# Kernel tuning notes

Hardware: AMD Instinct MI355X
Metric: run time of the kernel (lower is better)

The kernel has to match this reference:

```python
import jax, jax.numpy as jnp
import numpy as np

NUM_HEADS = 16
SIZE_PER_HEAD = 64
HIDDEN = NUM_HEADS * SIZE_PER_HEAD  # 1024
B, F, T = 4, 1024, 1024
NEG_INF = -10000.0


def setup_inputs() -> dict:
    key = jax.random.key(0)
    ks = jax.random.split(key, 6)
    scale = 0.02
    return {
        "from_tensor": jax.random.normal(ks[0], (B, F, HIDDEN), dtype=jnp.float32),
        "to_tensor": jax.random.normal(ks[1], (B, T, HIDDEN), dtype=jnp.float32),
        "attention_mask": jnp.ones((B, F, T), dtype=jnp.float32),
        "Wq": jax.random.normal(ks[2], (HIDDEN, HIDDEN), dtype=jnp.float32) * scale,
        "bq": jnp.zeros((HIDDEN,), dtype=jnp.float32),
        "Wk": jax.random.normal(ks[3], (HIDDEN, HIDDEN), dtype=jnp.float32) * scale,
        "bk": jnp.zeros((HIDDEN,), dtype=jnp.float32),
        "Wv": jax.random.normal(ks[4], (HIDDEN, HIDDEN), dtype=jnp.float32) * scale,
        "bv": jnp.zeros((HIDDEN,), dtype=jnp.float32),
    }


def _split_heads(x, seq_len):
    # [B, S, H*Dh] -> [B, H, S, Dh]
    return x.reshape(B, seq_len, NUM_HEADS, SIZE_PER_HEAD).transpose(0, 2, 1, 3)


def reference(from_tensor, to_tensor, attention_mask, Wq, bq, Wk, bk, Wv, bv):
    # Q/K/V dense projections (query_act/key_act/value_act are None -> linear)
    q = _split_heads(from_tensor @ Wq + bq, F)   # [B,H,F,Dh]
    k = _split_heads(to_tensor @ Wk + bk, T)     # [B,H,T,Dh]
    v = _split_heads(to_tensor @ Wv + bv, T)     # [B,H,T,Dh]

    # scaled dot-product attention scores: [B,H,F,T]
    scores = jnp.einsum("bhfd,bhtd->bhft", q, k) / jnp.sqrt(
        jnp.asarray(SIZE_PER_HEAD, dtype=q.dtype))

    # BERT-style mask adder: mask==1 -> attend, mask==0 -> -10000
    adder = (1.0 - attention_mask[:, None, :, :]) * NEG_INF
    scores = scores + adder

    attention_probs = jax.nn.softmax(scores, axis=-1)  # dropout_prob=0.0

    ctx = jnp.einsum("bhft,bhtd->bhfd", attention_probs, v)  # [B,H,F,Dh]
    ctx = ctx.transpose(0, 2, 1, 3).reshape(B, F, NUM_HEADS * SIZE_PER_HEAD)
    return ctx, attention_probs
```

## Files before the change

kernel.cpp:

```cpp
#include <hip/hip_runtime.h>

typedef unsigned short u16;
typedef __bf16 bf16x8 __attribute__((ext_vector_type(8)));
typedef float f32x4 __attribute__((ext_vector_type(4)));
typedef u16 u16x8 __attribute__((ext_vector_type(8)));
typedef u16 u16x4 __attribute__((ext_vector_type(4)));

#define NUM_HEADS 16
#define HIDDEN 1024
#define BATCH 4
#define SEQ 1024
#define C1 0.1803368809109783f
#define LOG2E 1.4426950408889634f

#define VMCNT0 asm volatile("s_waitcnt vmcnt(0)" ::: "memory")

static __device__ __forceinline__ u16 f2bf(float x) {
  unsigned u = __float_as_uint(x);
  u = u + 0x7FFFu + ((u >> 16) & 1u);
  return (u16)(u >> 16);
}
static __device__ __forceinline__ float bf2f(u16 b) {
  return __uint_as_float(((unsigned)b) << 16);
}
static __device__ __forceinline__ void async16(u16* lds, const u16* g) {
  __builtin_amdgcn_global_load_lds(
      (const __attribute__((address_space(1))) void*)g,
      (__attribute__((address_space(3))) void*)lds, 16, 0, 0);
}

__global__ __launch_bounds__(256) void k_prep(
    const float* __restrict__ from, u16* __restrict__ Af,
    const float* __restrict__ to, u16* __restrict__ At,
    const float* __restrict__ Wq, const float* __restrict__ Wk,
    const float* __restrict__ Wv, u16* __restrict__ Wt,
    const float* __restrict__ mask, u16* __restrict__ adder, int* __restrict__ flags) {
  int bid = blockIdx.x;
  int tid = threadIdx.x;
  if (bid < 4096) {
    const float* in = (bid < 2048) ? from : to;
    u16* out = (bid < 2048) ? Af : At;
    int i = (bid & 2047) * 256 + tid;
    float4 a = ((const float4*)in)[i * 2];
    float4 b = ((const float4*)in)[i * 2 + 1];
    u16x8 v;
    v[0] = f2bf(a.x); v[1] = f2bf(a.y); v[2] = f2bf(a.z); v[3] = f2bf(a.w);
    v[4] = f2bf(b.x); v[5] = f2bf(b.y); v[6] = f2bf(b.z); v[7] = f2bf(b.w);
    *(u16x8*)&out[(size_t)i * 8] = v;
  } else if (bid < 4864) {
    __shared__ float tile[64][65];
    int wid = bid - 4096;
    int z = wid >> 8, rem = wid & 255;
    int x = rem & 15, y = rem >> 4;
    const float* W = (z == 0) ? Wq : (z == 1) ? Wk : Wv;
    u16* out = Wt + (size_t)z * HIDDEN * HIDDEN;
    int k0 = y * 64, n0 = x * 64;
    int r = tid >> 6, c = tid & 63;
#pragma unroll
    for (int i = 0; i < 16; ++i)
      tile[i * 4 + r][c] = W[(size_t)(k0 + i * 4 + r) * HIDDEN + n0 + c];
    __syncthreads();
#pragma unroll
    for (int i = 0; i < 16; ++i)
      out[(size_t)(n0 + i * 4 + r) * HIDDEN + k0 + c] = f2bf(tile[c][i * 4 + r]);
  } else {
    int wid = bid - 4864;
    int tt = wid & 7, ft = (wid >> 3) & 7, b = wid >> 6;
    __shared__ int sflag;
    if (tid == 0) sflag = 0;
    __syncthreads();
    size_t base = ((size_t)b * SEQ + ft * 128) * SEQ + tt * 128;
    int any = 0;
#pragma unroll
    for (int i = 0; i < 16; ++i) {
      int idx = i * 256 + tid;
      int r = idx >> 5, c4 = idx & 31;
      float4 v = *(const float4*)&mask[base + (size_t)r * SEQ + c4 * 4];
      any |= (v.x != 1.0f) | (v.y != 1.0f) | (v.z != 1.0f) | (v.w != 1.0f);
    }
    if (any) sflag = 1;
    __syncthreads();
    if (sflag) {
#pragma unroll
      for (int i = 0; i < 16; ++i) {
        int idx = i * 256 + tid;
        int r = idx >> 5, c4 = idx & 31;
        float4 v = *(const float4*)&mask[base + (size_t)r * SEQ + c4 * 4];
        u16x4 o;
        o[0] = f2bf((1.0f - v.x) * -10000.0f * LOG2E);
        o[1] = f2bf((1.0f - v.y) * -10000.0f * LOG2E);
        o[2] = f2bf((1.0f - v.z) * -10000.0f * LOG2E);
        o[3] = f2bf((1.0f - v.w) * -10000.0f * LOG2E);
        *(u16x4*)&adder[base + (size_t)r * SEQ + c4 * 4] = o;
      }
    }
    if (tid == 0) flags[(b * 8 + ft) * 8 + tt] = sflag;
  }
}

__global__ __launch_bounds__(256) void k_gemmQKV(
    const u16* __restrict__ Af, const u16* __restrict__ At,
    const u16* __restrict__ Wt,
    const float* __restrict__ bq, const float* __restrict__ bk_, const float* __restrict__ bv_,
    u16* __restrict__ Qh, u16* __restrict__ Kh, u16* __restrict__ Vt) {
  __shared__ u16 lds[3 * 128 * 64];
  int bid = blockIdx.x;
  int which = bid >> 8;
  int wg = bid & 255;
  int xcd = wg & 7, j = wg >> 3;
  int ntile = j & 7, mstrip = xcd * 4 + (j >> 3);
  int m0 = mstrip * 128, n0 = ntile * 128;
  int tid = threadIdx.x, w = tid >> 6, lane = tid & 63;
  int wr = w >> 1, wc = w & 1;
  int g = lane >> 4, cc = lane & 15;

  int sx[4], srow[4], scol[4];
#pragma unroll
  for (int i = 0; i < 4; ++i) {
    int ch = w * 4 + i;
    int x = ch * 1024 + lane * 16;
    int row = x >> 7;
    int colb = (x & 127) ^ ((row & 7) << 4);
    sx[i] = ch * 512;
    srow[i] = row;
    scol[i] = colb >> 1;
  }

  if (which == 0) {
    u16* sA = lds;
    u16* sB = lds + 8192;
    const u16* A = Af;
    const u16* B = Wt;
    f32x4 acc[4][4] = {};

    for (int kt = 0; kt < HIDDEN / 64; ++kt) {
      __syncthreads();
#pragma unroll
      for (int i = 0; i < 4; ++i) {
        async16(&sA[sx[i]], A + (size_t)(m0 + srow[i]) * HIDDEN + kt * 64 + scol[i]);
        async16(&sB[sx[i]], B + (size_t)(n0 + srow[i]) * HIDDEN + kt * 64 + scol[i]);
      }
      VMCNT0;
      __syncthreads();
#pragma unroll
      for (int kk = 0; kk < 2; ++kk) {
        bf16x8 af[4], bfr[4];
#pragma unroll
        for (int mf = 0; mf < 4; ++mf) {
          int row = wr * 64 + mf * 16 + cc;
          int colb = (kk * 64 + (g << 4)) ^ ((row & 7) << 4);
          af[mf] = *(const bf16x8*)&sA[(row * 128 + colb) >> 1];
        }
#pragma unroll
        for (int nf = 0; nf < 4; ++nf) {
          int row = wc * 64 + nf * 16 + cc;
          int colb = (kk * 64 + (g << 4)) ^ ((row & 7) << 4);
          bfr[nf] = *(const bf16x8*)&sB[(row * 128 + colb) >> 1];
        }
#pragma unroll
        for (int mf = 0; mf < 4; ++mf)
#pragma unroll
          for (int nf = 0; nf < 4; ++nf)
            acc[mf][nf] = __builtin_amdgcn_mfma_f32_16x16x32_bf16(af[mf], bfr[nf], acc[mf][nf], 0, 0, 0);
      }
    }

#pragma unroll
    for (int mf = 0; mf < 4; ++mf) {
#pragma unroll
      for (int nf = 0; nf < 4; ++nf) {
        int n = n0 + wc * 64 + nf * 16 + cc;
        float bval = bq[n];
        int h = n >> 6, d = n & 63;
#pragma unroll
        for (int r = 0; r < 4; ++r) {
          int m = m0 + wr * 64 + mf * 16 + g * 4 + r;
          int b = m >> 10, s = m & 1023;
          Qh[((((size_t)b * NUM_HEADS + h) * SEQ + s) << 6) + d] = f2bf(acc[mf][nf][r] + bval);
        }
      }
    }
  } else {
    u16* sA = lds;
    u16* sBk = lds + 8192;
    u16* sBv = lds + 16384;
    const u16* Bk = Wt + (size_t)1 * HIDDEN * HIDDEN;
    const u16* Bv = Wt + (size_t)2 * HIDDEN * HIDDEN;
    f32x4 acck[4][4] = {};
    f32x4 accv[4][4] = {};

    for (int kt = 0; kt < HIDDEN / 64; ++kt) {
      __syncthreads();
#pragma unroll
      for (int i = 0; i < 4; ++i) {
        async16(&sA[sx[i]], At + (size_t)(m0 + srow[i]) * HIDDEN + kt * 64 + scol[i]);
        async16(&sBk[sx[i]], Bk + (size_t)(n0 + srow[i]) * HIDDEN + kt * 64 + scol[i]);
        async16(&sBv[sx[i]], Bv + (size_t)(n0 + srow[i]) * HIDDEN + kt * 64 + scol[i]);
      }
      VMCNT0;
      __syncthreads();
#pragma unroll
      for (int kk = 0; kk < 2; ++kk) {
        bf16x8 af[4], bkf[4], bvf[4];
#pragma unroll
        for (int mf = 0; mf < 4; ++mf) {
          int row = wr * 64 + mf * 16 + cc;
          int colb = (kk * 64 + (g << 4)) ^ ((row & 7) << 4);
          af[mf] = *(const bf16x8*)&sA[(row * 128 + colb) >> 1];
        }
#pragma unroll
        for (int nf = 0; nf < 4; ++nf) {
          int row = wc * 64 + nf * 16 + cc;
          int colb = (kk * 64 + (g << 4)) ^ ((row & 7) << 4);
          bkf[nf] = *(const bf16x8*)&sBk[(row * 128 + colb) >> 1];
          bvf[nf] = *(const bf16x8*)&sBv[(row * 128 + colb) >> 1];
        }
#pragma unroll
        for (int mf = 0; mf < 4; ++mf)
#pragma unroll
          for (int nf = 0; nf < 4; ++nf) {
            acck[mf][nf] = __builtin_amdgcn_mfma_f32_16x16x32_bf16(af[mf], bkf[nf], acck[mf][nf], 0, 0, 0);
            accv[mf][nf] = __builtin_amdgcn_mfma_f32_16x16x32_bf16(af[mf], bvf[nf], accv[mf][nf], 0, 0, 0);
          }
      }
    }

#pragma unroll
    for (int mf = 0; mf < 4; ++mf) {
#pragma unroll
      for (int nf = 0; nf < 4; ++nf) {
        int n = n0 + wc * 64 + nf * 16 + cc;
        float bval = bk_[n];
        int h = n >> 6, d = n & 63;
#pragma unroll
        for (int r = 0; r < 4; ++r) {
          int m = m0 + wr * 64 + mf * 16 + g * 4 + r;
          int b = m >> 10, s = m & 1023;
          Kh[((((size_t)b * NUM_HEADS + h) * SEQ + s) << 6) + d] = f2bf(acck[mf][nf][r] + bval);
        }
      }
    }

    __syncthreads();
    char* T = (char*)lds;
#pragma unroll
    for (int mf = 0; mf < 4; ++mf) {
#pragma unroll
      for (int nf = 0; nf < 4; ++nf) {
        int nl = wc * 64 + nf * 16 + cc;
        float bval = bv_[n0 + nl];
        int mlb = wr * 64 + mf * 16 + g * 4;
        u16x4 v;
#pragma unroll
        for (int r = 0; r < 4; ++r) v[r] = f2bf(accv[mf][nf][r] + bval);
        int byte = nl * 256 + ((mlb * 2) ^ ((nl & 7) << 4));
        *(u16x4*)(T + byte) = v;
      }
    }
    __syncthreads();
    int nl = tid >> 1, mh = (tid & 1) * 64;
    int b = m0 >> 10, s0 = m0 & 1023;
    u16* dst = &Vt[((size_t)b * 1024 + n0 + nl) * SEQ + s0 + mh];
#pragma unroll
    for (int j2 = 0; j2 < 8; ++j2) {
      int byte = nl * 256 + (((mh + j2 * 8) * 2) ^ ((nl & 7) << 4));
      *(u16x8*)&dst[j2 * 8] = *(const u16x8*)(T + byte);
    }
  }
}

__global__ __launch_bounds__(256, 3) void k_attn1(
    const u16* __restrict__ Qh, const u16* __restrict__ Kh,
    const u16* __restrict__ adder, const int* __restrict__ flags,
    float* __restrict__ invl) {
  __shared__ u16 sQ[128 * 64];
  __shared__ u16 sK[128 * 64];
  int ft = blockIdx.x, h = blockIdx.y, b = blockIdx.z;
  int f0 = ft * 128;
  int bh = b * NUM_HEADS + h;
  const u16* Qg = Qh + ((size_t)bh * SEQ + f0) * 64;
  const u16* Kg = Kh + (size_t)bh * SEQ * 64;
  int tid = threadIdx.x, w = tid >> 6, lane = tid & 63;
  int g = lane >> 4, cc = lane & 15;
  const int fbase = w * 32;

  int flgmask = 0;
#pragma unroll
  for (int tt = 0; tt < 8; ++tt)
    flgmask |= (flags[(b * 8 + ft) * 8 + tt] != 0) << tt;

  int sx[4], srow7[4], scol7[4];
#pragma unroll
  for (int i = 0; i < 4; ++i) {
    int ch = w * 4 + i;
    int x = ch * 1024 + lane * 16;
    sx[i] = ch * 512;
    int r7 = x >> 7;
    int c7 = (x & 127) ^ ((r7 & 7) << 4);
    srow7[i] = r7; scol7[i] = c7 >> 1;
  }

#pragma unroll
  for (int i = 0; i < 4; ++i)
    async16(&sQ[sx[i]], Qg + (size_t)srow7[i] * 64 + scol7[i]);

  float l_run[8];
#pragma unroll
  for (int i = 0; i < 8; ++i) l_run[i] = 0.0f;

  for (int tt = 0; tt < 8; ++tt) {
    __syncthreads();
#pragma unroll
    for (int i = 0; i < 4; ++i)
      async16(&sK[sx[i]], Kg + (size_t)(tt * 128 + srow7[i]) * 64 + scol7[i]);
    VMCNT0;
    __syncthreads();

    f32x4 s[2][8] = {};
#pragma unroll
    for (int kk = 0; kk < 2; ++kk) {
      bf16x8 aq[2], bk8[8];
#pragma unroll
      for (int mf = 0; mf < 2; ++mf) {
        int row = fbase + mf * 16 + cc;
        int colb = (kk * 64 + (g << 4)) ^ ((row & 7) << 4);
        aq[mf] = *(const bf16x8*)&sQ[(row * 128 + colb) >> 1];
      }
#pragma unroll
      for (int nf = 0; nf < 8; ++nf) {
        int row = nf * 16 + cc;
        int colb = (kk * 64 + (g << 4)) ^ ((row & 7) << 4);
        bk8[nf] = *(const bf16x8*)&sK[(row * 128 + colb) >> 1];
      }
#pragma unroll
      for (int mf = 0; mf < 2; ++mf)
#pragma unroll
        for (int nf = 0; nf < 8; ++nf)
          s[mf][nf] = __builtin_amdgcn_mfma_f32_16x16x32_bf16(aq[mf], bk8[nf], s[mf][nf], 0, 0, 0);
    }
#pragma unroll
    for (int mf = 0; mf < 2; ++mf)
#pragma unroll
      for (int nf = 0; nf < 8; ++nf)
        s[mf][nf] = s[mf][nf] * C1;
    if ((flgmask >> tt) & 1) {
      for (int mf = 0; mf < 2; ++mf)
        for (int nf = 0; nf < 8; ++nf)
          for (int r = 0; r < 4; ++r) {
            int frow = f0 + fbase + mf * 16 + g * 4 + r;
            int tcol = tt * 128 + nf * 16 + cc;
            s[mf][nf][r] += bf2f(adder[((size_t)b * SEQ + frow) * SEQ + tcol]);
          }
    }
#pragma unroll
    for (int mf = 0; mf < 2; ++mf)
#pragma unroll
      for (int r = 0; r < 4; ++r) {
        float sum = 0.f;
#pragma unroll
        for (int nf = 0; nf < 8; ++nf) sum += exp2f(s[mf][nf][r]);
        sum += __shfl_xor(sum, 1, 16);
        sum += __shfl_xor(sum, 2, 16);
        sum += __shfl_xor(sum, 4, 16);
        sum += __shfl_xor(sum, 8, 16);
        l_run[mf * 4 + r] += sum;
      }
  }

  if (cc == 0) {
#pragma unroll
    for (int mf = 0; mf < 2; ++mf)
#pragma unroll
      for (int r = 0; r < 4; ++r)
        invl[(size_t)bh * SEQ + f0 + fbase + mf * 16 + g * 4 + r] =
            1.0f / l_run[mf * 4 + r];
  }
}

__global__ __launch_bounds__(256) void k_attn2(
    const u16* __restrict__ Qh, const u16* __restrict__ Kh, const u16* __restrict__ Vt,
    const u16* __restrict__ adder, const int* __restrict__ flags,
    const float* __restrict__ invl,
    float* __restrict__ ctx, float* __restrict__ probs) {
  __shared__ u16 sQ[128 * 64];
  __shared__ u16 sK[128 * 64];
  __shared__ u16 sV[64 * 128];
  __shared__ u16 sP[128 * 128];
  int ft = blockIdx.x, h = blockIdx.y, b = blockIdx.z;
  int f0 = ft * 128;
  int bh = b * NUM_HEADS + h;
  const u16* Qg = Qh + ((size_t)bh * SEQ + f0) * 64;
  const u16* Kg = Kh + (size_t)bh * SEQ * 64;
  const u16* Vg = Vt + (size_t)bh * 64 * SEQ;
  int tid = threadIdx.x, w = tid >> 6, lane = tid & 63;
  int g = lane >> 4, cc = lane & 15;
  const int fbase = w * 32;

  int flgmask = 0;
#pragma unroll
  for (int tt = 0; tt < 8; ++tt)
    flgmask |= (flags[(b * 8 + ft) * 8 + tt] != 0) << tt;

  int sx[4], srow7[4], scol7[4], srow8[4], scol8[4];
#pragma unroll
  for (int i = 0; i < 4; ++i) {
    int ch = w * 4 + i;
    int x = ch * 1024 + lane * 16;
    sx[i] = ch * 512;
    int r7 = x >> 7;
    int c7 = (x & 127) ^ ((r7 & 7) << 4);
    srow7[i] = r7; scol7[i] = c7 >> 1;
    int r8 = x >> 8;
    int c8 = (x & 255) ^ ((r8 & 7) << 4);
    srow8[i] = r8; scol8[i] = c8 >> 1;
  }

#pragma unroll
  for (int i = 0; i < 4; ++i)
    async16(&sQ[sx[i]], Qg + (size_t)srow7[i] * 64 + scol7[i]);

  float inv_l[8];
#pragma unroll
  for (int mf = 0; mf < 2; ++mf)
#pragma unroll
    for (int r = 0; r < 4; ++r)
      inv_l[mf * 4 + r] =
          invl[(size_t)bh * SEQ + f0 + fbase + mf * 16 + g * 4 + r];

  f32x4 accO[2][4] = {};

  for (int tt = 0; tt < 8; ++tt) {
    __syncthreads();
#pragma unroll
    for (int i = 0; i < 4; ++i) {
      async16(&sK[sx[i]], Kg + (size_t)(tt * 128 + srow7[i]) * 64 + scol7[i]);
      async16(&sV[sx[i]], Vg + (size_t)srow8[i] * SEQ + tt * 128 + scol8[i]);
    }
    VMCNT0;
    __syncthreads();

    f32x4 s[2][8] = {};
#pragma unroll
    for (int kk = 0; kk < 2; ++kk) {
      bf16x8 aq[2], bk8[8];
#pragma unroll
      for (int mf = 0; mf < 2; ++mf) {
        int row = fbase + mf * 16 + cc;
        int colb = (kk * 64 + (g << 4)) ^ ((row & 7) << 4);
        aq[mf] = *(const bf16x8*)&sQ[(row * 128 + colb) >> 1];
      }
#pragma unroll
      for (int nf = 0; nf < 8; ++nf) {
        int row = nf * 16 + cc;
        int colb = (kk * 64 + (g << 4)) ^ ((row & 7) << 4);
        bk8[nf] = *(const bf16x8*)&sK[(row * 128 + colb) >> 1];
      }
#pragma unroll
      for (int mf = 0; mf < 2; ++mf)
#pragma unroll
        for (int nf = 0; nf < 8; ++nf)
          s[mf][nf] = __builtin_amdgcn_mfma_f32_16x16x32_bf16(aq[mf], bk8[nf], s[mf][nf], 0, 0, 0);
    }
#pragma unroll
    for (int mf = 0; mf < 2; ++mf)
#pragma unroll
      for (int nf = 0; nf < 8; ++nf)
        s[mf][nf] = s[mf][nf] * C1;
    if ((flgmask >> tt) & 1) {
      for (int mf = 0; mf < 2; ++mf)
        for (int nf = 0; nf < 8; ++nf)
          for (int r = 0; r < 4; ++r) {
            int frow = f0 + fbase + mf * 16 + g * 4 + r;
            int tcol = tt * 128 + nf * 16 + cc;
            s[mf][nf][r] += bf2f(adder[((size_t)b * SEQ + frow) * SEQ + tcol]);
          }
    }
#pragma unroll
    for (int mf = 0; mf < 2; ++mf)
#pragma unroll
      for (int nf = 0; nf < 8; ++nf)
#pragma unroll
        for (int r = 0; r < 4; ++r) {
          int idx = mf * 4 + r;
          float p = exp2f(s[mf][nf][r]) * inv_l[idx];
          int frow = fbase + mf * 16 + g * 4 + r;
          int tcol = nf * 16 + cc;
          probs[(((size_t)bh * SEQ) + f0 + frow) * SEQ + tt * 128 + tcol] = p;
          sP[(frow * 256 + ((tcol * 2) ^ ((frow & 7) << 4))) >> 1] = f2bf(p);
        }
#pragma unroll
    for (int ks = 0; ks < 4; ++ks) {
      bf16x8 ap[2], bv8[4];
#pragma unroll
      for (int mf = 0; mf < 2; ++mf) {
        int row = fbase + mf * 16 + cc;
        int colb = (ks * 64 + (g << 4)) ^ ((row & 7) << 4);
        ap[mf] = *(const bf16x8*)&sP[(row * 256 + colb) >> 1];
      }
#pragma unroll
      for (int nf = 0; nf < 4; ++nf) {
        int row = nf * 16 + cc;
        int colb = (ks * 64 + (g << 4)) ^ ((row & 7) << 4);
        bv8[nf] = *(const bf16x8*)&sV[(row * 256 + colb) >> 1];
      }
#pragma unroll
      for (int mf = 0; mf < 2; ++mf)
#pragma unroll
        for (int nf = 0; nf < 4; ++nf)
          accO[mf][nf] = __builtin_amdgcn_mfma_f32_16x16x32_bf16(ap[mf], bv8[nf], accO[mf][nf], 0, 0, 0);
    }
  }

#pragma unroll
  for (int mf = 0; mf < 2; ++mf)
#pragma unroll
    for (int nf = 0; nf < 4; ++nf)
#pragma unroll
      for (int r = 0; r < 4; ++r) {
        int frow = fbase + mf * 16 + g * 4 + r;
        int d = nf * 16 + cc;
        ctx[((size_t)b * SEQ + f0 + frow) * HIDDEN + h * 64 + d] = accO[mf][nf][r];
      }
}

extern "C" void kernel_launch(void* const* d_in, const int* in_sizes, int n_in,
                              void* d_out, int out_size, void* d_ws, size_t ws_size,
                              hipStream_t stream) {
  const float* from = (const float*)d_in[0];
  const float* to   = (const float*)d_in[1];
  const float* mask = (const float*)d_in[2];
  const float* Wq   = (const float*)d_in[3];
  const float* bq   = (const float*)d_in[4];
  const float* Wk   = (const float*)d_in[5];
  const float* bk   = (const float*)d_in[6];
  const float* Wv   = (const float*)d_in[7];
  const float* bv   = (const float*)d_in[8];

  char* ws = (char*)d_ws;
  u16* Af    = (u16*)(ws);
  u16* At    = (u16*)(ws + 8388608);
  u16* Wt    = (u16*)(ws + 16777216);
  u16* adder = (u16*)(ws + 23068672);
  int* flags = (int*)(ws + 31457280);
  u16* Qh    = (u16*)(ws + 31458304);
  u16* Kh    = (u16*)(ws + 39846912);
  u16* Vt    = (u16*)(ws + 48235520);
  float* invl = (float*)(ws);

  float* ctx = (float*)d_out;
  float* probs = ctx + (size_t)BATCH * SEQ * HIDDEN;

  k_prep<<<5120, 256, 0, stream>>>(from, Af, to, At, Wq, Wk, Wv, Wt, mask, adder, flags);
  k_gemmQKV<<<512, 256, 0, stream>>>(Af, At, Wt, bq, bk, bv, Qh, Kh, Vt);
  k_attn1<<<dim3(8, 16, 4), 256, 0, stream>>>(Qh, Kh, adder, flags, invl);
  k_attn2<<<dim3(8, 16, 4), 256, 0, stream>>>(Qh, Kh, Vt, adder, flags, invl, ctx, probs);
}
```

Before: 196.4 us.

## Split V projection out of QKV GEMM and co-schedule it with attention pass 1

The fused K+V GEMM blocks, which carried two accumulator sets and three LDS tiles, are split up. The first kernel now computes only Q and K, with one uniform code path. The V projection moves into the next launch, where 256 GEMM blocks run alongside the 512 row-sum (attn1) blocks that only need Q and K. This balances the per-block work and register use in the first GEMM and lets the V GEMM overlap with the softmax-denominator pass. The cost is that the combined kernel is bound by the attn1 launch bounds (3 blocks per CU), which may constrain registers for the GEMM branch.

```diff
diff --git a/kernel.cpp b/kernel.cpp
--- a/kernel.cpp
+++ b/kernel.cpp
@@ -98,14 +98,19 @@
   }
 }
 
-__global__ __launch_bounds__(256) void k_gemmQKV(
+__global__ __launch_bounds__(256) void k_gemmQK(
     const u16* __restrict__ Af, const u16* __restrict__ At,
     const u16* __restrict__ Wt,
-    const float* __restrict__ bq, const float* __restrict__ bk_, const float* __restrict__ bv_,
-    u16* __restrict__ Qh, u16* __restrict__ Kh, u16* __restrict__ Vt) {
-  __shared__ u16 lds[3 * 128 * 64];
+    const float* __restrict__ bq, const float* __restrict__ bk_,
+    u16* __restrict__ Qh, u16* __restrict__ Kh) {
+  __shared__ u16 sA[128 * 64];
+  __shared__ u16 sB[128 * 64];
   int bid = blockIdx.x;
   int which = bid >> 8;
+  const u16* A = which ? At : Af;
+  const u16* B = Wt + (size_t)which * HIDDEN * HIDDEN;
+  const float* bias = which ? bk_ : bq;
+  u16* out = which ? Kh : Qh;
   int wg = bid & 255;
   int xcd = wg & 7, j = wg >> 3;
   int ntile = j & 7, mstrip = xcd * 4 + (j >> 3);
@@ -113,6 +118,8 @@
   int tid = threadIdx.x, w = tid >> 6, lane = tid & 63;
   int wr = w >> 1, wc = w & 1;
   int g = lane >> 4, cc = lane & 15;
+
+  f32x4 acc[4][4] = {};
 
   int sx[4], srow[4], scol[4];
 #pragma unroll
@@ -126,168 +133,65 @@
     scol[i] = colb >> 1;
   }
 
-  if (which == 0) {
-    u16* sA = lds;
-    u16* sB = lds + 8192;
-    const u16* A = Af;
-    const u16* B = Wt;
-    f32x4 acc[4][4] = {};
-
-    for (int kt = 0; kt < HIDDEN / 64; ++kt) {
-      __syncthreads();
-#pragma unroll
-      for (int i = 0; i < 4; ++i) {
-        async16(&sA[sx[i]], A + (size_t)(m0 + srow[i]) * HIDDEN + kt * 64 + scol[i]);
-        async16(&sB[sx[i]], B + (size_t)(n0 + srow[i]) * HIDDEN + kt * 64 + scol[i]);
-      }
-      VMCNT0;
-      __syncthreads();
-#pragma unroll
-      for (int kk = 0; kk < 2; ++kk) {
-        bf16x8 af[4], bfr[4];
-#pragma unroll
-        for (int mf = 0; mf < 4; ++mf) {
-          int row = wr * 64 + mf * 16 + cc;
-          int colb = (kk * 64 + (g << 4)) ^ ((row & 7) << 4);
-          af[mf] = *(const bf16x8*)&sA[(row * 128 + colb) >> 1];
-        }
-#pragma unroll
-        for (int nf = 0; nf < 4; ++nf) {
-          int row = wc * 64 + nf * 16 + cc;
-          int colb = (kk * 64 + (g << 4)) ^ ((row & 7) << 4);
-          bfr[nf] = *(const bf16x8*)&sB[(row * 128 + colb) >> 1];
-        }
-#pragma unroll
-        for (int mf = 0; mf < 4; ++mf)
-#pragma unroll
-          for (int nf = 0; nf < 4; ++nf)
-            acc[mf][nf] = __builtin_amdgcn_mfma_f32_16x16x32_bf16(af[mf], bfr[nf], acc[mf][nf], 0, 0, 0);
-      }
-    }
-
-#pragma unroll
-    for (int mf = 0; mf < 4; ++mf) {
+  for (int kt = 0; kt < HIDDEN / 64; ++kt) {
+    __syncthreads();
+#pragma unroll
+    for (int i = 0; i < 4; ++i) {
+      async16(&sA[sx[i]], A + (size_t)(m0 + srow[i]) * HIDDEN + kt * 64 + scol[i]);
+      async16(&sB[sx[i]], B + (size_t)(n0 + srow[i]) * HIDDEN + kt * 64 + scol[i]);
+    }
+    VMCNT0;
+    __syncthreads();
+#pragma unroll
+    for (int kk = 0; kk < 2; ++kk) {
+      bf16x8 af[4], bfr[4];
+#pragma unroll
+      for (int mf = 0; mf < 4; ++mf) {
+        int row = wr * 64 + mf * 16 + cc;
+        int colb = (kk * 64 + (g << 4)) ^ ((row & 7) << 4);
+        af[mf] = *(const bf16x8*)&sA[(row * 128 + colb) >> 1];
+      }
 #pragma unroll
       for (int nf = 0; nf < 4; ++nf) {
-        int n = n0 + wc * 64 + nf * 16 + cc;
-        float bval = bq[n];
-        int h = n >> 6, d = n & 63;
-#pragma unroll
-        for (int r = 0; r < 4; ++r) {
-          int m = m0 + wr * 64 + mf * 16 + g * 4 + r;
-          int b = m >> 10, s = m & 1023;
-          Qh[((((size_t)b * NUM_HEADS + h) * SEQ + s) << 6) + d] = f2bf(acc[mf][nf][r] + bval);
-        }
-      }
-    }
-  } else {
-    u16* sA = lds;
-    u16* sBk = lds + 8192;
-    u16* sBv = lds + 16384;
-    const u16* Bk = Wt + (size_t)1 * HIDDEN * HIDDEN;
-    const u16* Bv = Wt + (size_t)2 * HIDDEN * HIDDEN;
-    f32x4 acck[4][4] = {};
-    f32x4 accv[4][4] = {};
-
-    for (int kt = 0; kt < HIDDEN / 64; ++kt) {
-      __syncthreads();
-#pragma unroll
-      for (int i = 0; i < 4; ++i) {
-        async16(&sA[sx[i]], At + (size_t)(m0 + srow[i]) * HIDDEN + kt * 64 + scol[i]);
-        async16(&sBk[sx[i]], Bk + (size_t)(n0 + srow[i]) * HIDDEN + kt * 64 + scol[i]);
-        async16(&sBv[sx[i]], Bv + (size_t)(n0 + srow[i]) * HIDDEN + kt * 64 + scol[i]);
-      }
-      VMCNT0;
-      __syncthreads();
-#pragma unroll
-      for (int kk = 0; kk < 2; ++kk) {
-        bf16x8 af[4], bkf[4], bvf[4];
-#pragma unroll
-        for (int mf = 0; mf < 4; ++mf) {
-          int row = wr * 64 + mf * 16 + cc;
-          int colb = (kk * 64 + (g << 4)) ^ ((row & 7) << 4);
-          af[mf] = *(const bf16x8*)&sA[(row * 128 + colb) >> 1];
-        }
-#pragma unroll
-        for (int nf = 0; nf < 4; ++nf) {
-          int row = wc * 64 + nf * 16 + cc;
-          int colb = (kk * 64 + (g << 4)) ^ ((row & 7) << 4);
-          bkf[nf] = *(const bf16x8*)&sBk[(row * 128 + colb) >> 1];
-          bvf[nf] = *(const bf16x8*)&sBv[(row * 128 + colb) >> 1];
-        }
-#pragma unroll
-        for (int mf = 0; mf < 4; ++mf)
-#pragma unroll
-          for (int nf = 0; nf < 4; ++nf) {
-            acck[mf][nf] = __builtin_amdgcn_mfma_f32_16x16x32_bf16(af[mf], bkf[nf], acck[mf][nf], 0, 0, 0);
-            accv[mf][nf] = __builtin_amdgcn_mfma_f32_16x16x32_bf16(af[mf], bvf[nf], accv[mf][nf], 0, 0, 0);
-          }
-      }
-    }
-
-#pragma unroll
-    for (int mf = 0; mf < 4; ++mf) {
-#pragma unroll
-      for (int nf = 0; nf < 4; ++nf) {
-        int n = n0 + wc * 64 + nf * 16 + cc;
-        float bval = bk_[n];
-        int h = n >> 6, d = n & 63;
-#pragma unroll
-        for (int r = 0; r < 4; ++r) {
-          int m = m0 + wr * 64 + mf * 16 + g * 4 + r;
-          int b = m >> 10, s = m & 1023;
-          Kh[((((size_t)b * NUM_HEADS + h) * SEQ + s) << 6) + d] = f2bf(acck[mf][nf][r] + bval);
-        }
-      }
-    }
-
-    __syncthreads();
-    char* T = (char*)lds;
-#pragma unroll
-    for (int mf = 0; mf < 4; ++mf) {
-#pragma unroll
-      for (int nf = 0; nf < 4; ++nf) {
-        int nl = wc * 64 + nf * 16 + cc;
-        float bval = bv_[n0 + nl];
-        int mlb = wr * 64 + mf * 16 + g * 4;
-        u16x4 v;
-#pragma unroll
-        for (int r = 0; r < 4; ++r) v[r] = f2bf(accv[mf][nf][r] + bval);
-        int byte = nl * 256 + ((mlb * 2) ^ ((nl & 7) << 4));
-        *(u16x4*)(T + byte) = v;
-      }
-    }
-    __syncthreads();
-    int nl = tid >> 1, mh = (tid & 1) * 64;
-    int b = m0 >> 10, s0 = m0 & 1023;
-    u16* dst = &Vt[((size_t)b * 1024 + n0 + nl) * SEQ + s0 + mh];
-#pragma unroll
-    for (int j2 = 0; j2 < 8; ++j2) {
-      int byte = nl * 256 + (((mh + j2 * 8) * 2) ^ ((nl & 7) << 4));
-      *(u16x8*)&dst[j2 * 8] = *(const u16x8*)(T + byte);
-    }
-  }
-}
-
-__global__ __launch_bounds__(256, 3) void k_attn1(
+        int row = wc * 64 + nf * 16 + cc;
+        int colb = (kk * 64 + (g << 4)) ^ ((row & 7) << 4);
+        bfr[nf] = *(const bf16x8*)&sB[(row * 128 + colb) >> 1];
+      }
+#pragma unroll
+      for (int mf = 0; mf < 4; ++mf)
+#pragma unroll
+        for (int nf = 0; nf < 4; ++nf)
+          acc[mf][nf] = __builtin_amdgcn_mfma_f32_16x16x32_bf16(af[mf], bfr[nf], acc[mf][nf], 0, 0, 0);
+    }
+  }
+
+#pragma unroll
+  for (int mf = 0; mf < 4; ++mf) {
+#pragma unroll
+    for (int nf = 0; nf < 4; ++nf) {
+      int n = n0 + wc * 64 + nf * 16 + cc;
+      float bval = bias[n];
+      int h = n >> 6, d = n & 63;
+#pragma unroll
+      for (int r = 0; r < 4; ++r) {
+        int m = m0 + wr * 64 + mf * 16 + g * 4 + r;
+        int b = m >> 10, s = m & 1023;
+        out[((((size_t)b * NUM_HEADS + h) * SEQ + s) << 6) + d] = f2bf(acc[mf][nf][r] + bval);
+      }
+    }
+  }
+}
+
+__global__ __launch_bounds__(256, 3) void k_gemmV_attn1(
+    const u16* __restrict__ At, const u16* __restrict__ Wt,
+    const float* __restrict__ bv_, u16* __restrict__ Vt,
     const u16* __restrict__ Qh, const u16* __restrict__ Kh,
     const u16* __restrict__ adder, const int* __restrict__ flags,
     float* __restrict__ invl) {
-  __shared__ u16 sQ[128 * 64];
-  __shared__ u16 sK[128 * 64];
-  int ft = blockIdx.x, h = blockIdx.y, b = blockIdx.z;
-  int f0 = ft * 128;
-  int bh = b * NUM_HEADS + h;
-  const u16* Qg = Qh + ((size_t)bh * SEQ + f0) * 64;
-  const u16* Kg = Kh + (size_t)bh * SEQ * 64;
+  __shared__ u16 lds[2 * 128 * 64];
+  int bid = blockIdx.x;
   int tid = threadIdx.x, w = tid >> 6, lane = tid & 63;
   int g = lane >> 4, cc = lane & 15;
-  const int fbase = w * 32;
-
-  int flgmask = 0;
-#pragma unroll
-  for (int tt = 0; tt < 8; ++tt)
-    flgmask |= (flags[(b * 8 + ft) * 8 + tt] != 0) << tt;
 
   int sx[4], srow7[4], scol7[4];
 #pragma unroll
@@ -300,80 +204,165 @@
     srow7[i] = r7; scol7[i] = c7 >> 1;
   }
 
-#pragma unroll
-  for (int i = 0; i < 4; ++i)
-    async16(&sQ[sx[i]], Qg + (size_t)srow7[i] * 64 + scol7[i]);
-
-  float l_run[8];
-#pragma unroll
-  for (int i = 0; i < 8; ++i) l_run[i] = 0.0f;
-
-  for (int tt = 0; tt < 8; ++tt) {
-    __syncthreads();
+  if (bid < 256) {
+    u16* sA = lds;
+    u16* sB = lds + 8192;
+    const u16* B = Wt + (size_t)2 * HIDDEN * HIDDEN;
+    int wg = bid;
+    int xcd = wg & 7, j = wg >> 3;
+    int ntile = j & 7, mstrip = xcd * 4 + (j >> 3);
+    int m0 = mstrip * 128, n0 = ntile * 128;
+    int wr = w >> 1, wc = w & 1;
+    f32x4 acc[4][4] = {};
+
+    for (int kt = 0; kt < HIDDEN / 64; ++kt) {
+      __syncthreads();
+#pragma unroll
+      for (int i = 0; i < 4; ++i) {
+        async16(&sA[sx[i]], At + (size_t)(m0 + srow7[i]) * HIDDEN + kt * 64 + scol7[i]);
+        async16(&sB[sx[i]], B + (size_t)(n0 + srow7[i]) * HIDDEN + kt * 64 + scol7[i]);
+      }
+      VMCNT0;
+      __syncthreads();
+#pragma unroll
+      for (int kk = 0; kk < 2; ++kk) {
+        bf16x8 af[4], bfr[4];
+#pragma unroll
+        for (int mf = 0; mf < 4; ++mf) {
+          int row = wr * 64 + mf * 16 + cc;
+          int colb = (kk * 64 + (g << 4)) ^ ((row & 7) << 4);
+          af[mf] = *(const bf16x8*)&sA[(row * 128 + colb) >> 1];
+        }
+#pragma unroll
+        for (int nf = 0; nf < 4; ++nf) {
+          int row = wc * 64 + nf * 16 + cc;
+          int colb = (kk * 64 + (g << 4)) ^ ((row & 7) << 4);
+          bfr[nf] = *(const bf16x8*)&sB[(row * 128 + colb) >> 1];
+        }
+#pragma unroll
+        for (int mf = 0; mf < 4; ++mf)
+#pragma unroll
+          for (int nf = 0; nf < 4; ++nf)
+            acc[mf][nf] = __builtin_amdgcn_mfma_f32_16x16x32_bf16(af[mf], bfr[nf], acc[mf][nf], 0, 0, 0);
+      }
+    }
+
+    __syncthreads();
+    char* T = (char*)lds;
+#pragma unroll
+    for (int mf = 0; mf < 4; ++mf) {
+#pragma unroll
+      for (int nf = 0; nf < 4; ++nf) {
+        int nl = wc * 64 + nf * 16 + cc;
+        float bval = bv_[n0 + nl];
+        int mlb = wr * 64 + mf * 16 + g * 4;
+        u16x4 v;
+#pragma unroll
+        for (int r = 0; r < 4; ++r) v[r] = f2bf(acc[mf][nf][r] + bval);
+        int byte = nl * 256 + ((mlb * 2) ^ ((nl & 7) << 4));
+        *(u16x4*)(T + byte) = v;
+      }
+    }
+    __syncthreads();
+    int nl = tid >> 1, mh = (tid & 1) * 64;
+    int b = m0 >> 10, s0 = m0 & 1023;
+    u16* dst = &Vt[((size_t)b * 1024 + n0 + nl) * SEQ + s0 + mh];
+#pragma unroll
+    for (int j2 = 0; j2 < 8; ++j2) {
+      int byte = nl * 256 + (((mh + j2 * 8) * 2) ^ ((nl & 7) << 4));
+      *(u16x8*)&dst[j2 * 8] = *(const u16x8*)(T + byte);
+    }
+  } else {
+    u16* sQ = lds;
+    u16* sK = lds + 8192;
+    int wid = bid - 256;
+    int ft = wid & 7, h = (wid >> 3) & 15, b = wid >> 7;
+    int f0 = ft * 128;
+    int bh = b * NUM_HEADS + h;
+    const u16* Qg = Qh + ((size_t)bh * SEQ + f0) * 64;
+    const u16* Kg = Kh + (size_t)bh * SEQ * 64;
+    const int fbase = w * 32;
+
+    int flgmask = 0;
+#pragma unroll
+    for (int tt = 0; tt < 8; ++tt)
+      flgmask |= (flags[(b * 8 + ft) * 8 + tt] != 0) << tt;
+
 #pragma unroll
     for (int i = 0; i < 4; ++i)
-      async16(&sK[sx[i]], Kg + (size_t)(tt * 128 + srow7[i]) * 64 + scol7[i]);
-    VMCNT0;
-    __syncthreads();
-
-    f32x4 s[2][8] = {};
-#pragma unroll
-    for (int kk = 0; kk < 2; ++kk) {
-      bf16x8 aq[2], bk8[8];
-#pragma unroll
-      for (int mf = 0; mf < 2; ++mf) {
-        int row = fbase + mf * 16 + cc;
-        int colb = (kk * 64 + (g << 4)) ^ ((row & 7) << 4);
-        aq[mf] = *(const bf16x8*)&sQ[(row * 128 + colb) >> 1];
-      }
-#pragma unroll
-      for (int nf = 0; nf < 8; ++nf) {
-        int row = nf * 16 + cc;
-        int colb = (kk * 64 + (g << 4)) ^ ((row & 7) << 4);
-        bk8[nf] = *(const bf16x8*)&sK[(row * 128 + colb) >> 1];
+      async16(&sQ[sx[i]], Qg + (size_t)srow7[i] * 64 + scol7[i]);
+
+    float l_run[8];
+#pragma unroll
+    for (int i = 0; i < 8; ++i) l_run[i] = 0.0f;
+
+    for (int tt = 0; tt < 8; ++tt) {
+      __syncthreads();
+#pragma unroll
+      for (int i = 0; i < 4; ++i)
+        async16(&sK[sx[i]], Kg + (size_t)(tt * 128 + srow7[i]) * 64 + scol7[i]);
+      VMCNT0;
+      __syncthreads();
+
+      f32x4 s[2][8] = {};
+#pragma unroll
+      for (int kk = 0; kk < 2; ++kk) {
+        bf16x8 aq[2], bk8[8];
+#pragma unroll
+        for (int mf = 0; mf < 2; ++mf) {
+          int row = fbase + mf * 16 + cc;
+          int colb = (kk * 64 + (g << 4)) ^ ((row & 7) << 4);
+          aq[mf] = *(const bf16x8*)&sQ[(row * 128 + colb) >> 1];
+        }
+#pragma unroll
+        for (int nf = 0; nf < 8; ++nf) {
+          int row = nf * 16 + cc;
+          int colb = (kk * 64 + (g << 4)) ^ ((row & 7) << 4);
+          bk8[nf] = *(const bf16x8*)&sK[(row * 128 + colb) >> 1];
+        }
+#pragma unroll
+        for (int mf = 0; mf < 2; ++mf)
+#pragma unroll
+          for (int nf = 0; nf < 8; ++nf)
+            s[mf][nf] = __builtin_amdgcn_mfma_f32_16x16x32_bf16(aq[mf], bk8[nf], s[mf][nf], 0, 0, 0);
       }
 #pragma unroll
       for (int mf = 0; mf < 2; ++mf)
 #pragma unroll
         for (int nf = 0; nf < 8; ++nf)
-          s[mf][nf] = __builtin_amdgcn_mfma_f32_16x16x32_bf16(aq[mf], bk8[nf], s[mf][nf], 0, 0, 0);
-    }
-#pragma unroll
-    for (int mf = 0; mf < 2; ++mf)
-#pragma unroll
-      for (int nf = 0; nf < 8; ++nf)
-        s[mf][nf] = s[mf][nf] * C1;
-    if ((flgmask >> tt) & 1) {
+          s[mf][nf] = s[mf][nf] * C1;
+      if ((flgmask >> tt) & 1) {
+        for (int mf = 0; mf < 2; ++mf)
+          for (int nf = 0; nf < 8; ++nf)
+            for (int r = 0; r < 4; ++r) {
+              int frow = f0 + fbase + mf * 16 + g * 4 + r;
+              int tcol = tt * 128 + nf * 16 + cc;
+              s[mf][nf][r] += bf2f(adder[((size_t)b * SEQ + frow) * SEQ + tcol]);
+            }
+      }
+#pragma unroll
       for (int mf = 0; mf < 2; ++mf)
-        for (int nf = 0; nf < 8; ++nf)
-          for (int r = 0; r < 4; ++r) {
-            int frow = f0 + fbase + mf * 16 + g * 4 + r;
-            int tcol = tt * 128 + nf * 16 + cc;
-            s[mf][nf][r] += bf2f(adder[((size_t)b * SEQ + frow) * SEQ + tcol]);
-          }
-    }
-#pragma unroll
-    for (int mf = 0; mf < 2; ++mf)
-#pragma unroll
-      for (int r = 0; r < 4; ++r) {
-        float sum = 0.f;
-#pragma unroll
-        for (int nf = 0; nf < 8; ++nf) sum += exp2f(s[mf][nf][r]);
-        sum += __shfl_xor(sum, 1, 16);
-        sum += __shfl_xor(sum, 2, 16);
-        sum += __shfl_xor(sum, 4, 16);
-        sum += __shfl_xor(sum, 8, 16);
-        l_run[mf * 4 + r] += sum;
-      }
-  }
-
-  if (cc == 0) {
-#pragma unroll
-    for (int mf = 0; mf < 2; ++mf)
-#pragma unroll
-      for (int r = 0; r < 4; ++r)
-        invl[(size_t)bh * SEQ + f0 + fbase + mf * 16 + g * 4 + r] =
-            1.0f / l_run[mf * 4 + r];
+#pragma unroll
+        for (int r = 0; r < 4; ++r) {
+          float sum = 0.f;
+#pragma unroll
+          for (int nf = 0; nf < 8; ++nf) sum += exp2f(s[mf][nf][r]);
+          sum += __shfl_xor(sum, 1, 16);
+          sum += __shfl_xor(sum, 2, 16);
+          sum += __shfl_xor(sum, 4, 16);
+          sum += __shfl_xor(sum, 8, 16);
+          l_run[mf * 4 + r] += sum;
+        }
+    }
+
+    if (cc == 0) {
+#pragma unroll
+      for (int mf = 0; mf < 2; ++mf)
+#pragma unroll
+        for (int r = 0; r < 4; ++r)
+          invl[(size_t)bh * SEQ + f0 + fbase + mf * 16 + g * 4 + r] =
+              1.0f / l_run[mf * 4 + r];
+    }
   }
 }
 
@@ -551,7 +540,7 @@
   float* probs = ctx + (size_t)BATCH * SEQ * HIDDEN;
 
   k_prep<<<5120, 256, 0, stream>>>(from, Af, to, At, Wq, Wk, Wv, Wt, mask, adder, flags);
-  k_gemmQKV<<<512, 256, 0, stream>>>(Af, At, Wt, bq, bk, bv, Qh, Kh, Vt);
-  k_attn1<<<dim3(8, 16, 4), 256, 0, stream>>>(Qh, Kh, adder, flags, invl);
+  k_gemmQK<<<512, 256, 0, stream>>>(Af, At, Wt, bq, bk, Qh, Kh);
+  k_gemmV_attn1<<<768, 256, 0, stream>>>(At, Wt, bv, Vt, Qh, Kh, adder, flags, invl);
   k_attn2<<<dim3(8, 16, 4), 256, 0, stream>>>(Qh, Kh, Vt, adder, flags, invl, ctx, probs);
 }
```

Measured after the change: 172.5 us (median of 3 runs). 1.14x faster.
